# Performance work log

Measured on AMD Instinct MI355X. Metric: run time of the kernel, lower is better.

Reference implementation:

```python
import jax, jax.numpy as jnp
import numpy as np

SPD = 24


def setup_inputs() -> dict:
    key = jax.random.key(0)
    k1, k2 = jax.random.split(key)
    x = jax.random.normal(k1, (128, 1024, 768), dtype=jnp.float32)
    # stand-in for orthogonally-initialized projection weight [spd_dim, in_dim]
    W = jax.random.normal(k2, (SPD, 768), dtype=jnp.float32) / np.float32(np.sqrt(768.0))
    return {"x": x, "W": W}


def reference(x, W):
    # projection: nn.Linear(bias=False) -> x @ W.T, [B, T, spd]
    p = jnp.einsum('btd,kd->btk', x, W)
    p = p - jnp.mean(p, axis=1, keepdims=True)
    n = p.shape[1]
    # covariance [B, spd, spd]
    cov = jnp.einsum('btk,btl->bkl', p, p) / (n - 1 + 1e-6)
    trace = jnp.trace(cov, axis1=-2, axis2=-1)[:, None, None]
    cov = cov / (trace + 1e-6)
    cov = (cov + jnp.swapaxes(cov, -1, -2)) / 2
    cov = cov + 1e-4 * jnp.eye(SPD, dtype=cov.dtype)
    eig_vals, eig_vecs = jnp.linalg.eigh(cov)
    log_vals = jnp.log(jnp.clip(eig_vals, 1e-6))
    # V diag(log_vals) V^T
    log_cov = jnp.einsum('bik,bk,bjk->bij', eig_vecs, log_vals, eig_vecs)
    iu, ju = jnp.triu_indices(SPD)
    return log_cov[:, iu, ju]  # [B, spd*(spd+1)/2]
```

## Files before the change

kernel.cpp:

```cpp
#include <hip/hip_runtime.h>
#include <math.h>


#define B_      128
#define T_      1024
#define D_      768
#define K_      24
#define ROWS    256
#define BPB     4
#define DCHUNK  32
#define NLD     8
#define LSTRIDE 36
#define PSTRIDE 28
#define NACC    600
#define NPAIR   300
#define SWEEPS  10

__global__ __launch_bounds__(256, 2) void socpool_proj(
    const float* __restrict__ x, const float* __restrict__ W,
    float* __restrict__ partial) {
  __shared__ float smem[ROWS * LSTRIDE];
  const int tid = threadIdx.x;
  const int b  = blockIdx.x >> 2;
  const int rb = blockIdx.x & 3;
  const float* xbase = x + ((size_t)b * T_ + rb * ROWS) * D_;
  const int r0 = tid >> 3;
  const int j4 = (tid & 7) * 4;
  const float* gp = xbase + (size_t)r0 * D_ + j4;
  const int lbase = r0 * LSTRIDE + j4;

  float acc[K_];
#pragma unroll
  for (int k = 0; k < K_; ++k) acc[k] = 0.f;

  float4 pre[NLD];
#pragma unroll
  for (int it = 0; it < NLD; ++it)
    pre[it] = *(const float4*)(gp + (size_t)it * 32 * D_);

  for (int dc = 0; dc < D_; dc += DCHUNK) {
    __syncthreads();
#pragma unroll
    for (int it = 0; it < NLD; ++it)
      *(float4*)(&smem[lbase + it * 32 * LSTRIDE]) = pre[it];
    __syncthreads();
    if (dc + DCHUNK < D_) {
#pragma unroll
      for (int it = 0; it < NLD; ++it)
        pre[it] = *(const float4*)(gp + (dc + DCHUNK) + (size_t)it * 32 * D_);
    }
#pragma unroll
    for (int d = 0; d < DCHUNK; d += 4) {
      float4 xv = *(const float4*)(&smem[tid * LSTRIDE + d]);
      const float* wp = W + dc + d;
#pragma unroll
      for (int k = 0; k < K_; ++k) {
        const float* wr = wp + (size_t)k * D_;
        acc[k] = fmaf(xv.x, wr[0], acc[k]);
        acc[k] = fmaf(xv.y, wr[1], acc[k]);
        acc[k] = fmaf(xv.z, wr[2], acc[k]);
        acc[k] = fmaf(xv.w, wr[3], acc[k]);
      }
    }
  }
  __syncthreads();
  float* P = smem;
#pragma unroll
  for (int q = 0; q < 6; ++q)
    *(float4*)(&P[tid * PSTRIDE + 4 * q]) =
        make_float4(acc[4*q], acc[4*q+1], acc[4*q+2], acc[4*q+3]);
  __syncthreads();
  float* outp = partial + (size_t)blockIdx.x * NACC;
  if (tid < 144) {
    const int k = tid / 6;
    const int q = (tid % 6) * 4;
    float a0=0.f,a1=0.f,a2=0.f,a3=0.f,b0=0.f,b1=0.f,b2=0.f,b3=0.f;
    for (int t = 0; t < ROWS; t += 2) {
      float  pk0 = P[t * PSTRIDE + k];
      float4 pq0 = *(const float4*)(&P[t * PSTRIDE + q]);
      float  pk1 = P[(t + 1) * PSTRIDE + k];
      float4 pq1 = *(const float4*)(&P[(t + 1) * PSTRIDE + q]);
      a0 = fmaf(pk0, pq0.x, a0); a1 = fmaf(pk0, pq0.y, a1);
      a2 = fmaf(pk0, pq0.z, a2); a3 = fmaf(pk0, pq0.w, a3);
      b0 = fmaf(pk1, pq1.x, b0); b1 = fmaf(pk1, pq1.y, b1);
      b2 = fmaf(pk1, pq1.z, b2); b3 = fmaf(pk1, pq1.w, b3);
    }
    outp[k * K_ + q + 0] = a0 + b0;
    outp[k * K_ + q + 1] = a1 + b1;
    outp[k * K_ + q + 2] = a2 + b2;
    outp[k * K_ + q + 3] = a3 + b3;
  } else if (tid < 168) {
    const int k = tid - 144;
    float s0 = 0.f, s1 = 0.f;
    for (int t = 0; t < ROWS; t += 2) {
      s0 += P[t * PSTRIDE + k];
      s1 += P[(t + 1) * PSTRIDE + k];
    }
    outp[576 + k] = s0 + s1;
  }
}

__global__ __launch_bounds__(64, 1) void socpool_eig(
    const float* __restrict__ partial, float* __restrict__ out) {
  __shared__ float Amat[K_ * 25];
  __shared__ float Qs[K_ * 25];
  __shared__ float lv[K_];
  __shared__ float raw[NACC];
  const int tid = threadIdx.x;
  const int b = blockIdx.x;

#pragma unroll
  for (int i = 0; i < 10; ++i) {
    int e = tid + (i << 6);
    if (e < NACC) {
      float v = 0.f;
#pragma unroll
      for (int jj = 0; jj < BPB; ++jj)
        v += partial[(size_t)(b * BPB + jj) * NACC + e];
      raw[e] = v;
    }
  }
  __syncthreads();

  const float inv_n   = 1.f / 1024.f;
  const float inv_nm1 = 1.f / (1023.f + 1e-6f);
  float cv[9];
#pragma unroll
  for (int i = 0; i < 9; ++i) {
    int e = tid + (i << 6);
    int k = e / K_, l = e % K_;
    cv[i] = (raw[e] - raw[576 + k] * raw[576 + l] * inv_n) * inv_nm1;
    Amat[k * 25 + l] = cv[i];
  }
  __syncthreads();
  float tr = 0.f;
#pragma unroll
  for (int k = 0; k < K_; ++k) tr += Amat[k * 25 + k];
  float sym[9];
#pragma unroll
  for (int i = 0; i < 9; ++i) {
    int e = tid + (i << 6);
    int k = e / K_, l = e % K_;
    sym[i] = cv[i] + Amat[l * 25 + k];
  }
  __syncthreads();
  const float sc = 0.5f / (tr + 1e-6f);
#pragma unroll
  for (int i = 0; i < 9; ++i) {
    int e = tid + (i << 6);
    int k = e / K_, l = e % K_;
    Amat[k * 25 + l] = sym[i] * sc + ((k == l) ? 1e-4f : 0.f);
  }
  __syncthreads();

  const int j = tid;
  float G[K_];
#pragma unroll
  for (int r = 0; r < K_; ++r)
    G[r] = (j < K_) ? Amat[r * 25 + j] : 0.f;

  float nn = 0.f;
  for (int sweep = 0; sweep < SWEEPS; ++sweep) {
    {
      float n0=0.f,n1=0.f,n2=0.f,n3=0.f;
#pragma unroll
      for (int r = 0; r < K_; r += 4) {
        n0 = fmaf(G[r],   G[r],   n0);
        n1 = fmaf(G[r+1], G[r+1], n1);
        n2 = fmaf(G[r+2], G[r+2], n2);
        n3 = fmaf(G[r+3], G[r+3], n3);
      }
      nn = (n0 + n1) + (n2 + n3);
    }
    float offacc = 0.f;
    for (int rr = 0; rr < 23; ++rr) {
      int partner;
      if (j == 23) {
        partner = (12 * rr) % 23;
      } else if (j < 23) {
        partner = rr - j;
        if (partner < 0) partner += 23;
        if (partner == j) partner = 23;
      } else {
        partner = j;
      }
      float oth[K_];
#pragma unroll
      for (int r = 0; r < K_; ++r) oth[r] = __shfl(G[r], partner, 64);
      float d0=0.f,d1=0.f,d2=0.f,d3=0.f;
#pragma unroll
      for (int r = 0; r < K_; r += 4) {
        d0 = fmaf(G[r],   oth[r],   d0);
        d1 = fmaf(G[r+1], oth[r+1], d1);
        d2 = fmaf(G[r+2], oth[r+2], d2);
        d3 = fmaf(G[r+3], oth[r+3], d3);
      }
      float gpq = (d0 + d1) + (d2 + d3);
      float nno = __shfl(nn, partner, 64);
      const bool low = (j < partner);
      float app = low ? nn : nno;
      float aqq = low ? nno : nn;
      float t = 0.f, cc = 1.f, ss = 0.f;
      if (j != partner && fabsf(gpq) > 1e-30f) {
        float tau = (aqq - app) / (2.f * gpq);
        t = 1.f / (fabsf(tau) + sqrtf(1.f + tau * tau));
        if (tau < 0.f) t = -t;
        cc = 1.f / sqrtf(1.f + t * t);
        ss = t * cc;
      }
      float sg = low ? -ss : ss;
#pragma unroll
      for (int r = 0; r < K_; ++r) G[r] = fmaf(sg, oth[r], cc * G[r]);
      nn += low ? (-t * gpq) : (t * gpq);
      if (j < K_) offacc += gpq * gpq;
    }
#pragma unroll
    for (int m = 1; m < 64; m <<= 1) offacc += __shfl_xor(offacc, m, 64);
    if (offacc < 1e-12f) break;
  }

  if (j < K_) {
    float n0=0.f,n1=0.f;
#pragma unroll
    for (int r = 0; r < K_; r += 2) {
      n0 = fmaf(G[r],   G[r],   n0);
      n1 = fmaf(G[r+1], G[r+1], n1);
    }
    float lam = sqrtf(n0 + n1);
    lv[j] = logf(fmaxf(lam, 1e-6f));
    float inv = 1.f / fmaxf(lam, 1e-20f);
#pragma unroll
    for (int r = 0; r < K_; ++r) Qs[r * 25 + j] = G[r] * inv;
  }
  __syncthreads();

  for (int e = tid; e < NPAIR; e += 64) {
    int i = 0, base = 0;
    while (i < K_ - 1 && base + (K_ - i) <= e) { base += K_ - i; ++i; }
    int jj = i + (e - base);
    float sum = 0.f;
#pragma unroll
    for (int k = 0; k < K_; ++k)
      sum = fmaf(Qs[i * 25 + k] * lv[k], Qs[jj * 25 + k], sum);
    out[(size_t)b * NPAIR + e] = sum;
  }
}

extern "C" void kernel_launch(void* const* d_in, const int* in_sizes, int n_in,
                              void* d_out, int out_size, void* d_ws, size_t ws_size,
                              hipStream_t stream) {
  const float* x = (const float*)d_in[0];
  const float* W = (const float*)d_in[1];
  float* partial = (float*)d_ws;
  float* out = (float*)d_out;
  hipLaunchKernelGGL(socpool_proj, dim3(B_ * BPB), dim3(256), 0, stream,
                     x, W, partial);
  hipLaunchKernelGGL(socpool_eig, dim3(B_), dim3(64), 0, stream,
                     partial, out);
}
```

Before: 884.5 us.

## Stream x via async global-to-LDS loads and rework Jacobi eigensolver exchange

The projection kernel now uses global_load_lds to stream x chunks directly into a double-buffered, XOR-swizzled LDS tile, replacing the register prefetch and store-to-LDS. This is meant to cut VGPR pressure and the extra LDS write pass. The eigen kernel now swaps columns through LDS instead of 24 shuffles and recomputes norms each rotation. It also drops the early convergence check and lowers the sweep cap to 8, which may cost accuracy on matrices that converge slowly.

```diff
diff --git a/kernel.cpp b/kernel.cpp
--- a/kernel.cpp
+++ b/kernel.cpp
@@ -1,6 +1,9 @@
 #include <hip/hip_runtime.h>
 #include <math.h>
 
+
+#define AS1 __attribute__((address_space(1)))
+#define AS3 __attribute__((address_space(3)))
 
 #define B_      128
 #define T_      1024
@@ -9,50 +12,51 @@
 #define ROWS    256
 #define BPB     4
 #define DCHUNK  32
-#define NLD     8
-#define LSTRIDE 36
+#define CHW     8192
 #define PSTRIDE 28
 #define NACC    600
 #define NPAIR   300
-#define SWEEPS  10
+#define SWEEPS  8
 
 __global__ __launch_bounds__(256, 2) void socpool_proj(
     const float* __restrict__ x, const float* __restrict__ W,
     float* __restrict__ partial) {
-  __shared__ float smem[ROWS * LSTRIDE];
-  const int tid = threadIdx.x;
-  const int b  = blockIdx.x >> 2;
-  const int rb = blockIdx.x & 3;
+  __shared__ float smem[2 * CHW];
+  const int tid  = threadIdx.x;
+  const int b    = blockIdx.x >> 2;
+  const int rb   = blockIdx.x & 3;
+  const int wv   = tid >> 6;
+  const int lane = tid & 63;
   const float* xbase = x + ((size_t)b * T_ + rb * ROWS) * D_;
-  const int r0 = tid >> 3;
-  const int j4 = (tid & 7) * 4;
-  const float* gp = xbase + (size_t)r0 * D_ + j4;
-  const int lbase = r0 * LSTRIDE + j4;
 
   float acc[K_];
 #pragma unroll
   for (int k = 0; k < K_; ++k) acc[k] = 0.f;
 
-  float4 pre[NLD];
-#pragma unroll
-  for (int it = 0; it < NLD; ++it)
-    pre[it] = *(const float4*)(gp + (size_t)it * 32 * D_);
-
-  for (int dc = 0; dc < D_; dc += DCHUNK) {
-    __syncthreads();
-#pragma unroll
-    for (int it = 0; it < NLD; ++it)
-      *(float4*)(&smem[lbase + it * 32 * LSTRIDE]) = pre[it];
-    __syncthreads();
-    if (dc + DCHUNK < D_) {
-#pragma unroll
-      for (int it = 0; it < NLD; ++it)
-        pre[it] = *(const float4*)(gp + (dc + DCHUNK) + (size_t)it * 32 * D_);
-    }
-#pragma unroll
-    for (int d = 0; d < DCHUNK; d += 4) {
-      float4 xv = *(const float4*)(&smem[tid * LSTRIDE + d]);
-      const float* wp = W + dc + d;
+  auto issue = [&](int dc, int bufsel) {
+    float* buf = smem + bufsel * CHW;
+#pragma unroll
+    for (int it = 0; it < 8; ++it) {
+      const int fl  = it * 256 + wv * 64 + lane;
+      const int row = fl >> 3;
+      const int qlg = (fl & 7) ^ (row & 7);
+      const float* g = xbase + (size_t)row * D_ + (dc + (qlg << 2));
+      float* l = buf + (size_t)(it * 256 + wv * 64) * 4;
+      __builtin_amdgcn_global_load_lds((const AS1 void*)g, (AS3 void*)l,
+                                       16, 0, 0);
+    }
+  };
+
+  issue(0, 0);
+  __syncthreads();
+  for (int c = 0; c < D_ / DCHUNK; ++c) {
+    if (c + 1 < D_ / DCHUNK) issue((c + 1) * DCHUNK, (c + 1) & 1);
+    const float* buf = smem + (c & 1) * CHW;
+    const int dc = c * DCHUNK;
+#pragma unroll
+    for (int qd = 0; qd < 8; ++qd) {
+      float4 xv = *(const float4*)(&buf[tid * 32 + ((qd ^ (tid & 7)) << 2)]);
+      const float* wp = W + dc + (qd << 2);
 #pragma unroll
       for (int k = 0; k < K_; ++k) {
         const float* wr = wp + (size_t)k * D_;
@@ -62,8 +66,9 @@
         acc[k] = fmaf(xv.w, wr[3], acc[k]);
       }
     }
-  }
-  __syncthreads();
+    __syncthreads();
+  }
+
   float* P = smem;
 #pragma unroll
   for (int q = 0; q < 6; ++q)
@@ -106,6 +111,7 @@
   __shared__ float Qs[K_ * 25];
   __shared__ float lv[K_];
   __shared__ float raw[NACC];
+  __shared__ float Xc[K_ * PSTRIDE];
   const int tid = threadIdx.x;
   const int b = blockIdx.x;
 
@@ -154,25 +160,16 @@
   __syncthreads();
 
   const int j = tid;
-  float G[K_];
-#pragma unroll
-  for (int r = 0; r < K_; ++r)
-    G[r] = (j < K_) ? Amat[r * 25 + j] : 0.f;
-
-  float nn = 0.f;
+  float4 Gv[6];
+#pragma unroll
+  for (int q = 0; q < 6; ++q) {
+    Gv[q].x = (j < K_) ? Amat[j * 25 + 4*q + 0] : 0.f;
+    Gv[q].y = (j < K_) ? Amat[j * 25 + 4*q + 1] : 0.f;
+    Gv[q].z = (j < K_) ? Amat[j * 25 + 4*q + 2] : 0.f;
+    Gv[q].w = (j < K_) ? Amat[j * 25 + 4*q + 3] : 0.f;
+  }
+
   for (int sweep = 0; sweep < SWEEPS; ++sweep) {
-    {
-      float n0=0.f,n1=0.f,n2=0.f,n3=0.f;
-#pragma unroll
-      for (int r = 0; r < K_; r += 4) {
-        n0 = fmaf(G[r],   G[r],   n0);
-        n1 = fmaf(G[r+1], G[r+1], n1);
-        n2 = fmaf(G[r+2], G[r+2], n2);
-        n3 = fmaf(G[r+3], G[r+3], n3);
-      }
-      nn = (n0 + n1) + (n2 + n3);
-    }
-    float offacc = 0.f;
     for (int rr = 0; rr < 23; ++rr) {
       int partner;
       if (j == 23) {
@@ -184,53 +181,72 @@
       } else {
         partner = j;
       }
-      float oth[K_];
-#pragma unroll
-      for (int r = 0; r < K_; ++r) oth[r] = __shfl(G[r], partner, 64);
-      float d0=0.f,d1=0.f,d2=0.f,d3=0.f;
-#pragma unroll
-      for (int r = 0; r < K_; r += 4) {
-        d0 = fmaf(G[r],   oth[r],   d0);
-        d1 = fmaf(G[r+1], oth[r+1], d1);
-        d2 = fmaf(G[r+2], oth[r+2], d2);
-        d3 = fmaf(G[r+3], oth[r+3], d3);
-      }
-      float gpq = (d0 + d1) + (d2 + d3);
-      float nno = __shfl(nn, partner, 64);
+      if (j < K_) {
+#pragma unroll
+        for (int q = 0; q < 6; ++q)
+          *(float4*)(&Xc[j * PSTRIDE + (q << 2)]) = Gv[q];
+      }
+      __syncthreads();
+      const int pcol = (partner < K_) ? partner : 0;
+      float4 O[6];
+#pragma unroll
+      for (int q = 0; q < 6; ++q)
+        O[q] = *(const float4*)(&Xc[pcol * PSTRIDE + (q << 2)]);
+      float a0=0.f,a1=0.f,a2=0.f,a3=0.f;
+      float b0=0.f,b1=0.f,b2=0.f,b3=0.f;
+      float c0=0.f,c1=0.f,c2=0.f,c3=0.f;
+#pragma unroll
+      for (int q = 0; q < 6; ++q) {
+        a0 = fmaf(Gv[q].x, Gv[q].x, a0); a1 = fmaf(Gv[q].y, Gv[q].y, a1);
+        a2 = fmaf(Gv[q].z, Gv[q].z, a2); a3 = fmaf(Gv[q].w, Gv[q].w, a3);
+        b0 = fmaf(O[q].x, O[q].x, b0);   b1 = fmaf(O[q].y, O[q].y, b1);
+        b2 = fmaf(O[q].z, O[q].z, b2);   b3 = fmaf(O[q].w, O[q].w, b3);
+        c0 = fmaf(Gv[q].x, O[q].x, c0);  c1 = fmaf(Gv[q].y, O[q].y, c1);
+        c2 = fmaf(Gv[q].z, O[q].z, c2);  c3 = fmaf(Gv[q].w, O[q].w, c3);
+      }
+      float nn  = (a0 + a1) + (a2 + a3);
+      float nno = (b0 + b1) + (b2 + b3);
+      float gpq = (c0 + c1) + (c2 + c3);
       const bool low = (j < partner);
       float app = low ? nn : nno;
       float aqq = low ? nno : nn;
-      float t = 0.f, cc = 1.f, ss = 0.f;
+      float cc = 1.f, ss = 0.f;
       if (j != partner && fabsf(gpq) > 1e-30f) {
         float tau = (aqq - app) / (2.f * gpq);
-        t = 1.f / (fabsf(tau) + sqrtf(1.f + tau * tau));
+        float t = 1.f / (fabsf(tau) + sqrtf(1.f + tau * tau));
         if (tau < 0.f) t = -t;
         cc = 1.f / sqrtf(1.f + t * t);
         ss = t * cc;
       }
       float sg = low ? -ss : ss;
 #pragma unroll
-      for (int r = 0; r < K_; ++r) G[r] = fmaf(sg, oth[r], cc * G[r]);
-      nn += low ? (-t * gpq) : (t * gpq);
-      if (j < K_) offacc += gpq * gpq;
-    }
-#pragma unroll
-    for (int m = 1; m < 64; m <<= 1) offacc += __shfl_xor(offacc, m, 64);
-    if (offacc < 1e-12f) break;
+      for (int q = 0; q < 6; ++q) {
+        Gv[q].x = fmaf(sg, O[q].x, cc * Gv[q].x);
+        Gv[q].y = fmaf(sg, O[q].y, cc * Gv[q].y);
+        Gv[q].z = fmaf(sg, O[q].z, cc * Gv[q].z);
+        Gv[q].w = fmaf(sg, O[q].w, cc * Gv[q].w);
+      }
+      __syncthreads();
+    }
   }
 
   if (j < K_) {
-    float n0=0.f,n1=0.f;
-#pragma unroll
-    for (int r = 0; r < K_; r += 2) {
-      n0 = fmaf(G[r],   G[r],   n0);
-      n1 = fmaf(G[r+1], G[r+1], n1);
-    }
-    float lam = sqrtf(n0 + n1);
+    float n0=0.f,n1=0.f,n2=0.f,n3=0.f;
+#pragma unroll
+    for (int q = 0; q < 6; ++q) {
+      n0 = fmaf(Gv[q].x, Gv[q].x, n0); n1 = fmaf(Gv[q].y, Gv[q].y, n1);
+      n2 = fmaf(Gv[q].z, Gv[q].z, n2); n3 = fmaf(Gv[q].w, Gv[q].w, n3);
+    }
+    float lam = sqrtf((n0 + n1) + (n2 + n3));
     lv[j] = logf(fmaxf(lam, 1e-6f));
     float inv = 1.f / fmaxf(lam, 1e-20f);
 #pragma unroll
-    for (int r = 0; r < K_; ++r) Qs[r * 25 + j] = G[r] * inv;
+    for (int q = 0; q < 6; ++q) {
+      Qs[(4*q + 0) * 25 + j] = Gv[q].x * inv;
+      Qs[(4*q + 1) * 25 + j] = Gv[q].y * inv;
+      Qs[(4*q + 2) * 25 + j] = Gv[q].z * inv;
+      Qs[(4*q + 3) * 25 + j] = Gv[q].w * inv;
+    }
   }
   __syncthreads();
 
```

New measurement: 876.7 us. Within noise of the previous version (-0.9%).
